# Performance work log

Hardware: AMD Instinct MI355X
Metric: run time of the kernel (lower is better)

## Reference

```python
import jax, jax.numpy as jnp
import numpy as np

IGNORE_THRESH = 0.75
COORD_SCALE = 1.0
NOOBJ_SCALE = 1.0
OBJ_SCALE = 5.0
CLASS_SCALE = 1.0


def setup_inputs() -> dict:
    key = jax.random.key(0)
    k1, k2, k3, k4, k5 = jax.random.split(key, 5)
    B, A, C, S, M = 32, 5, 20, 52, 50
    outputs = jax.random.normal(k1, (B, A * (5 + C), S, S), dtype=jnp.float32) * 0.5
    # targets: [x_c, y_c, w, h, conf, class] with normalized coords in (0,1)
    xy = jax.random.uniform(k2, (B, M, 2), minval=0.1, maxval=0.9)
    wh = jax.random.uniform(k3, (B, M, 2), minval=0.02, maxval=0.25)
    cls = jax.random.randint(k4, (B, M, 1), 0, C).astype(jnp.float32)
    conf = jnp.ones((B, M, 1), dtype=jnp.float32)
    targets = jnp.concatenate([xy, wh, conf, cls], axis=-1).astype(jnp.float32)
    anchors = jnp.array([[1.3221, 1.73145], [3.19275, 4.00944], [5.05587, 8.09892],
                         [9.47112, 4.84053], [11.2364, 10.0071]], dtype=jnp.float32)
    return {"outputs": outputs, "targets": targets, "anchors": anchors}


def _iou_xywh(a, b):
    # a: [B, N, 4], b: [B, M, 4] (cx, cy, w, h) -> [B, N, M]
    tl = jnp.maximum(a[:, :, None, :2] - a[:, :, None, 2:] * 0.5,
                     b[:, None, :, :2] - b[:, None, :, 2:] * 0.5)
    br = jnp.minimum(a[:, :, None, :2] + a[:, :, None, 2:] * 0.5,
                     b[:, None, :, :2] + b[:, None, :, 2:] * 0.5)
    en = jnp.all(tl < br, axis=-1).astype(a.dtype)
    area_i = jnp.prod(br - tl, axis=-1) * en
    area_a = a[:, :, 2] * a[:, :, 3]
    area_b = b[:, :, 2] * b[:, :, 3]
    return area_i / (area_a[:, :, None] + area_b[:, None, :] - area_i)


def _yolo_loss(outputs, targets, anchors):
    B, Ct, S, _ = outputs.shape
    A = anchors.shape[0]
    nc = Ct // A - 5
    dt = outputs.dtype
    out = outputs.reshape(B, A, 5 + nc, S, S).transpose(0, 1, 3, 4, 2)  # B,A,S,S,D

    # ---- decode predicted boxes (grid units) ----
    xs = jnp.arange(S, dtype=dt)
    px = jax.nn.sigmoid(out[..., 0]) + xs[None, None, None, :]
    py = jax.nn.sigmoid(out[..., 1]) + xs[None, None, :, None]
    pw = jnp.exp(out[..., 2]) * anchors[:, 0][None, :, None, None]
    ph = jnp.exp(out[..., 3]) * anchors[:, 1][None, :, None, None]
    # cell-major ordering: (S*S, A)
    pred_boxes = jnp.stack([px, py, pw, ph], -1).transpose(0, 2, 3, 1, 4).reshape(B, S * S * A, 4)

    valid = targets.sum(-1) > 0                      # [B,M]
    gt = targets[..., :4] * S                        # [B,M,4] grid units
    gcls = targets[..., 5].astype(jnp.int32)         # [B,M]

    # ---- pred-vs-gt IoU, ignore mask ----
    ious = _iou_xywh(pred_boxes, gt)                 # [B, S*S*A, M]
    ious = jnp.where(valid[:, None, :], ious, 0.0)
    max_iou = ious.max(-1).reshape(B, S * S, A)      # [B,S*S,A]
    iou_mask = jnp.where(max_iou >= IGNORE_THRESH, 0.0, NOOBJ_SCALE).astype(dt)

    # ---- per-gt responsible cell & anchor ----
    gx, gy, gw, gh = gt[..., 0], gt[..., 1], gt[..., 2], gt[..., 3]
    cx = jnp.clip(jnp.floor(gx - gw * 0.5), 0, S - 1).astype(jnp.int32)
    cy = jnp.clip(jnp.floor(gy - gh * 0.5), 0, S - 1).astype(jnp.int32)
    cell = cy * S + cx                               # [B,M]
    acx = cx.astype(dt) + 0.5
    acy = cy.astype(dt) + 0.5
    aw, ah = anchors[:, 0], anchors[:, 1]            # [A]
    # anchor-vs-gt IoU at the responsible cell: [B,M,A]
    tlx = jnp.maximum(acx[..., None] - aw * 0.5, (gx - gw * 0.5)[..., None])
    brx = jnp.minimum(acx[..., None] + aw * 0.5, (gx + gw * 0.5)[..., None])
    tly = jnp.maximum(acy[..., None] - ah * 0.5, (gy - gh * 0.5)[..., None])
    bry = jnp.minimum(acy[..., None] + ah * 0.5, (gy + gh * 0.5)[..., None])
    en = ((tlx < brx) & (tly < bry)).astype(dt)
    inter = (brx - tlx) * (bry - tly) * en
    aiou = inter / (aw * ah + (gw * gh)[..., None] - inter)
    best = jnp.argmax(aiou, -1)                      # [B,M]

    # deltas sigma(tx), sigma(ty), exp(tw), exp(th)
    deltas = jnp.stack([gx - acx, gy - acy, gw / aw[best], gh / ah[best]], -1)  # [B,M,4]

    b_idx = jnp.broadcast_to(jnp.arange(B)[:, None], cell.shape)
    cell_sc = jnp.where(valid, cell, S * S)          # OOB -> dropped on scatter
    miou = max_iou[b_idx, cell, best]                # [B,M]

    box_target = jnp.zeros((B, S * S, A, 4), dt).at[b_idx, cell_sc, best].set(deltas)
    box_mask = jnp.zeros((B, S * S, A), dt).at[b_idx, cell_sc, best].set(1.0)
    class_target = jnp.zeros((B, S * S, A), jnp.int32).at[b_idx, cell_sc, best].set(gcls)
    class_mask = jnp.zeros((B, S * S, A), dt).at[b_idx, cell_sc, best].set(1.0)
    iou_target = jnp.zeros((B, S * S, A), dt).at[b_idx, cell_sc, best].set(miou)
    iou_mask = iou_mask.at[b_idx, cell_sc, best].set(OBJ_SCALE)

    # ---- losses (cell-major predictions) ----
    pr = out.transpose(0, 2, 3, 1, 4).reshape(B, S * S, A, 5 + nc)
    pred_delta = jnp.concatenate([jax.nn.sigmoid(pr[..., :2]), jnp.exp(pr[..., 2:4])], -1)
    pconf = jax.nn.sigmoid(pr[..., 4])
    logp = jax.nn.log_softmax(pr[..., 5:], axis=-1)

    Bf = jnp.asarray(B, dt)
    box_loss = COORD_SCALE * jnp.sum(box_mask[..., None] * (pred_delta - box_target) ** 2) / (2.0 * Bf)
    iou_loss = jnp.sum((iou_mask * (pconf - iou_target)) ** 2) / (2.0 * Bf)
    nll = -jnp.take_along_axis(logp, class_target[..., None], axis=-1)[..., 0]
    class_loss = CLASS_SCALE * jnp.sum(class_mask * nll) / Bf
    return box_loss + iou_loss + class_loss


def reference(outputs, targets, anchors):
    return _yolo_loss(outputs, targets, anchors)
```

## Files before the change

### kernel.cpp

```cpp
#include <hip/hip_runtime.h>
#include <math.h>

namespace {
constexpr int S  = 52;
constexpr int SS = S * S;
constexpr int A  = 5;
constexpr int NC = 20;
constexpr int CH = 5 + NC;
constexpr int B  = 32;
constexpr int M  = 50;
constexpr int TSTRIDE = 6;
constexpr float IGNORE_T = 0.75f;
constexpr float C37 = 3.0f / 7.0f;

constexpr int POS_PER_T = 4;
constexpr int CHUNK = 256 * POS_PER_T;
constexpr int NBY = (SS + CHUNK - 1) / CHUNK;
constexpr int NBA = B * A;
constexpr int NBLK_NOOBJ = NBA * NBY;
constexpr int NBLK = NBLK_NOOBJ + B;
constexpr int Q4 = SS / 4;

__device__ __forceinline__ float sigm(float x) { return 1.0f / (1.0f + __expf(-x)); }

__device__ __forceinline__ float iou_one(float px, float py, float pw, float ph,
                                         float gx, float gy, float gw, float gh) {
  float tlx = fmaxf(px - pw * 0.5f, gx - gw * 0.5f);
  float brx = fminf(px + pw * 0.5f, gx + gw * 0.5f);
  float tly = fmaxf(py - ph * 0.5f, gy - gh * 0.5f);
  float bry = fminf(py + ph * 0.5f, gy + gh * 0.5f);
  if (tlx < brx && tly < bry) {
    float ai = (brx - tlx) * (bry - tly);
    return ai / (pw * ph + gw * gh - ai);
  }
  return 0.0f;
}

__global__ __launch_bounds__(256) void k_fused(const float* __restrict__ outp,
                                               const float* __restrict__ targ,
                                               const float* __restrict__ anch,
                                               float* __restrict__ out) {
  __shared__ float4 sgc[M];
  __shared__ float  sga[M];
  __shared__ float  sg[M][4];
  __shared__ int    sv[M];
  __shared__ int    skey[64];
  __shared__ float  wsum[4];

  const int bid = blockIdx.x;
  const int tid = threadIdx.x;

  if (bid < NBLK_NOOBJ) {
    const int ba = bid % NBA;
    const int by = bid / NBA;
    const int b  = ba / A, a = ba % A;
    if (tid < M) {
      const float* t = targ + (size_t)(b * M + tid) * TSTRIDE;
      float t0 = t[0], t1 = t[1], t2 = t[2], t3 = t[3], t4 = t[4], t5 = t[5];
      bool valid = (t0 + t1 + t2 + t3 + t4 + t5) > 0.0f;
      float gx = t0 * S, gy = t1 * S, gw = t2 * S, gh = t3 * S;
      if (valid) {
        sgc[tid] = make_float4(gx - gw * 0.5f, gy - gh * 0.5f,
                               gx + gw * 0.5f, gy + gh * 0.5f);
        sga[tid] = C37 * gw * gh;
      } else {
        sgc[tid] = make_float4(1e30f, 1e30f, -1e30f, -1e30f);
        sga[tid] = 0.0f;
      }
    }
    __syncthreads();

    const float aw = anch[2 * a], ah = anch[2 * a + 1];
    int q = by * (CHUNK / 4) + tid;
    const bool act = q < Q4;
    if (!act) q = Q4 - 1;
    const float4* p0 = (const float4*)(outp + (size_t)ba * CH * SS);
    float4 tx4 = p0[q];
    float4 ty4 = p0[q + Q4];
    float4 tw4 = p0[q + 2 * Q4];
    float4 th4 = p0[q + 3 * Q4];
    float4 tc4 = p0[q + 4 * Q4];

    const int pos0 = q * 4;
    const int y = pos0 / S, x0 = pos0 - y * S;
    const float fy = (float)y;

    float ptlx[POS_PER_T], ptly[POS_PER_T], pbrx[POS_PER_T], pbry[POS_PER_T];
    float rhsb[POS_PER_T], pcsq[POS_PER_T];
    const float txx[4] = {tx4.x, tx4.y, tx4.z, tx4.w};
    const float tyy[4] = {ty4.x, ty4.y, ty4.z, ty4.w};
    const float tww[4] = {tw4.x, tw4.y, tw4.z, tw4.w};
    const float thh[4] = {th4.x, th4.y, th4.z, th4.w};
    const float tcc[4] = {tc4.x, tc4.y, tc4.z, tc4.w};
#pragma unroll
    for (int k = 0; k < POS_PER_T; ++k) {
      float px = sigm(txx[k]) + (float)(x0 + k);
      float py = sigm(tyy[k]) + fy;
      float pw = __expf(tww[k]) * aw;
      float ph = __expf(thh[k]) * ah;
      float hw = pw * 0.5f, hh = ph * 0.5f;
      ptlx[k] = px - hw;
      ptly[k] = py - hh;
      pbrx[k] = px + hw;
      pbry[k] = py + hh;
      rhsb[k] = C37 * (pw * ph);
      float pc = sigm(tcc[k]);
      pcsq[k] = act ? pc * pc : 0.0f;
    }

    for (int m = 0; m < M; ++m) {
      float4 g = sgc[m];
      float ga = sga[m];
#pragma unroll
      for (int k = 0; k < POS_PER_T; ++k) {
        float dx = fminf(pbrx[k], g.z) - fmaxf(ptlx[k], g.x);
        float dy = fminf(pbry[k], g.w) - fmaxf(ptly[k], g.y);
        float ai = dx * dy;
        bool hit = (fminf(dx, dy) > 0.0f) & (ai >= rhsb[k] + ga);
        pcsq[k] = hit ? 0.0f : pcsq[k];
      }
    }

    float term = (pcsq[0] + pcsq[1]) + (pcsq[2] + pcsq[3]);
    for (int off = 32; off > 0; off >>= 1) term += __shfl_down(term, off);
    int lane = tid & 63, wid = tid >> 6;
    if (lane == 0) wsum[wid] = term;
    __syncthreads();
    if (tid == 0)
      atomicAdd(out, (wsum[0] + wsum[1] + wsum[2] + wsum[3]) * (1.0f / 64.0f));
  } else {
    const int b = bid - NBLK_NOOBJ;
    const int m = tid;
    int valid = 0;
    float gx = 0, gy = 0, gw = 0, gh = 0;
    int gcls = 0, cx = 0, cy = 0, best = 0;
    float dxv = 0, dyv = 0, dwv = 0, dhv = 0;
    if (m < M) {
      const float* t = targ + (size_t)(b * M + m) * TSTRIDE;
      float t0 = t[0], t1 = t[1], t2 = t[2], t3 = t[3], t4 = t[4], t5 = t[5];
      valid = (t0 + t1 + t2 + t3 + t4 + t5) > 0.0f ? 1 : 0;
      gx = t0 * S; gy = t1 * S; gw = t2 * S; gh = t3 * S;
      gcls = (int)t5;
      sg[m][0] = gx; sg[m][1] = gy; sg[m][2] = gw; sg[m][3] = gh;
      sv[m] = valid;
    }
    if (valid) {
      cx = (int)fminf(fmaxf(floorf(gx - gw * 0.5f), 0.0f), (float)(S - 1));
      cy = (int)fminf(fmaxf(floorf(gy - gh * 0.5f), 0.0f), (float)(S - 1));
      float acx = cx + 0.5f, acy = cy + 0.5f;
      float bestv = -1.0f;
      for (int k = 0; k < A; ++k) {
        float aw = anch[2 * k], ah = anch[2 * k + 1];
        float tlx = fmaxf(acx - aw * 0.5f, gx - gw * 0.5f);
        float brx = fminf(acx + aw * 0.5f, gx + gw * 0.5f);
        float tly = fmaxf(acy - ah * 0.5f, gy - gh * 0.5f);
        float bry = fminf(acy + ah * 0.5f, gy + gh * 0.5f);
        float v = 0.0f;
        if (tlx < brx && tly < bry) {
          float ai = (brx - tlx) * (bry - tly);
          v = ai / (aw * ah + gw * gh - ai);
        }
        if (v > bestv) { bestv = v; best = k; }
      }
      dxv = gx - acx; dyv = gy - acy;
      dwv = gw / anch[2 * best]; dhv = gh / anch[2 * best + 1];
    }
    if (m < 64) skey[m] = valid ? ((cy * S + cx) * A + best) : -1;
    __syncthreads();
    bool winner = (valid != 0);
    if (winner) {
      int key = skey[m];
      for (int mm = m + 1; mm < M; ++mm)
        if (skey[mm] == key) { winner = false; break; }
    }
    float ciou = 0.0f, cbox = 0.0f, ccls = 0.0f;
    if (winner) {
      int cell = cy * S + cx;
      const float* base = outp + (size_t)(b * A + best) * CH * SS + cell;
      float tx = base[0], ty = base[SS], tw = base[2 * SS], th = base[3 * SS], tc = base[4 * SS];
      float aw = anch[2 * best], ah = anch[2 * best + 1];
      float px = sigm(tx) + (float)cx;
      float py = sigm(ty) + (float)cy;
      float pw = __expf(tw) * aw;
      float ph = __expf(th) * ah;
      float miou = 0.0f;
      for (int mm = 0; mm < M; ++mm)
        if (sv[mm])
          miou = fmaxf(miou, iou_one(px, py, pw, ph,
                                     sg[mm][0], sg[mm][1], sg[mm][2], sg[mm][3]));
      float pc = sigm(tc);
      float defterm = (miou >= IGNORE_T) ? 0.0f : pc * pc;
      float d5 = 5.0f * (pc - miou);
      ciou = d5 * d5 - defterm;
      float e0 = sigm(tx) - dxv;
      float e1 = sigm(ty) - dyv;
      float e2 = __expf(tw) - dwv;
      float e3 = __expf(th) - dhv;
      cbox = e0 * e0 + e1 * e1 + e2 * e2 + e3 * e3;
      float l[NC];
      float lmax = -1e30f;
      for (int c = 0; c < NC; ++c) { l[c] = base[(5 + c) * SS]; lmax = fmaxf(lmax, l[c]); }
      float se = 0.0f;
      for (int c = 0; c < NC; ++c) se += __expf(l[c] - lmax);
      ccls = (lmax + __logf(se)) - l[gcls];
    }
    if (m < 64) {
      for (int off = 32; off > 0; off >>= 1) {
        ciou += __shfl_down(ciou, off);
        cbox += __shfl_down(cbox, off);
        ccls += __shfl_down(ccls, off);
      }
      if (m == 0)
        atomicAdd(out, (ciou + cbox) * (1.0f / 64.0f) + ccls * (1.0f / 32.0f));
    }
  }
}

}

extern "C" void kernel_launch(void* const* d_in, const int* in_sizes, int n_in,
                              void* d_out, int out_size, void* d_ws, size_t ws_size,
                              hipStream_t stream) {
  const float* outp = (const float*)d_in[0];
  const float* targ = (const float*)d_in[1];
  const float* anch = (const float*)d_in[2];

  hipMemsetAsync(d_out, 0, 4, stream);
  k_fused<<<NBLK, 256, 0, stream>>>(outp, targ, anch, (float*)d_out);
}
```

Before: 31.38 us.

## Replace memset and global atomics with flag-based last-block reduction in block zero

Removes the separate hipMemsetAsync on the output and the 512 atomicAdds that all hit one address. Each producer block now writes its partial sum to a workspace slot and publishes a release flag. Block 0 spin-waits on all 512 flags, reduces the partials, writes the result directly and resets the flags. This saves a launch and the atomic contention. In exchange it relies on every block being co-resident or making progress while block 0 spins, and on the workspace flags starting out not equal to the magic value.

```diff
diff --git a/kernel.cpp b/kernel.cpp
--- a/kernel.cpp
+++ b/kernel.cpp
@@ -18,8 +18,10 @@
 constexpr int NBY = (SS + CHUNK - 1) / CHUNK;
 constexpr int NBA = B * A;
 constexpr int NBLK_NOOBJ = NBA * NBY;
-constexpr int NBLK = NBLK_NOOBJ + B;
+constexpr int NPROD = NBLK_NOOBJ + B;
+constexpr int NBLK = NPROD + 1;
 constexpr int Q4 = SS / 4;
+constexpr unsigned MAGIC = 0x5F3759DFu;
 
 __device__ __forceinline__ float sigm(float x) { return 1.0f / (1.0f + __expf(-x)); }
 
@@ -36,9 +38,18 @@
   return 0.0f;
 }
 
+__device__ __forceinline__ void publish(float* partials, unsigned* flags, int p,
+                                        float v) {
+  partials[p] = v;
+  __threadfence();
+  __hip_atomic_store(&flags[p], MAGIC, __ATOMIC_RELEASE, __HIP_MEMORY_SCOPE_AGENT);
+}
+
 __global__ __launch_bounds__(256) void k_fused(const float* __restrict__ outp,
                                                const float* __restrict__ targ,
                                                const float* __restrict__ anch,
+                                               float* __restrict__ partials,
+                                               unsigned* __restrict__ flags,
                                                float* __restrict__ out) {
   __shared__ float4 sgc[M];
   __shared__ float  sga[M];
@@ -50,9 +61,34 @@
   const int bid = blockIdx.x;
   const int tid = threadIdx.x;
 
-  if (bid < NBLK_NOOBJ) {
-    const int ba = bid % NBA;
-    const int by = bid / NBA;
+  if (bid == 0) {
+    const int i0 = tid, i1 = tid + 256;
+    while (__hip_atomic_load(&flags[i0], __ATOMIC_ACQUIRE,
+                             __HIP_MEMORY_SCOPE_AGENT) != MAGIC)
+      __builtin_amdgcn_s_sleep(2);
+    while (__hip_atomic_load(&flags[i1], __ATOMIC_ACQUIRE,
+                             __HIP_MEMORY_SCOPE_AGENT) != MAGIC)
+      __builtin_amdgcn_s_sleep(2);
+    float s = __hip_atomic_load(&partials[i0], __ATOMIC_RELAXED,
+                                __HIP_MEMORY_SCOPE_AGENT) +
+              __hip_atomic_load(&partials[i1], __ATOMIC_RELAXED,
+                                __HIP_MEMORY_SCOPE_AGENT);
+    for (int off = 32; off > 0; off >>= 1) s += __shfl_down(s, off);
+    int lane = tid & 63, wid = tid >> 6;
+    if (lane == 0) wsum[wid] = s;
+    __syncthreads();
+    if (tid == 0)
+      out[0] = wsum[0] + wsum[1] + wsum[2] + wsum[3];
+    __hip_atomic_store(&flags[i0], 0u, __ATOMIC_RELAXED, __HIP_MEMORY_SCOPE_AGENT);
+    __hip_atomic_store(&flags[i1], 0u, __ATOMIC_RELAXED, __HIP_MEMORY_SCOPE_AGENT);
+    return;
+  }
+
+  const int p = bid - 1;
+
+  if (p < NBLK_NOOBJ) {
+    const int ba = p % NBA;
+    const int by = p / NBA;
     const int b  = ba / A, a = ba % A;
     if (tid < M) {
       const float* t = targ + (size_t)(b * M + tid) * TSTRIDE;
@@ -127,9 +163,10 @@
     if (lane == 0) wsum[wid] = term;
     __syncthreads();
     if (tid == 0)
-      atomicAdd(out, (wsum[0] + wsum[1] + wsum[2] + wsum[3]) * (1.0f / 64.0f));
+      publish(partials, flags, p,
+              (wsum[0] + wsum[1] + wsum[2] + wsum[3]) * (1.0f / 64.0f));
   } else {
-    const int b = bid - NBLK_NOOBJ;
+    const int b = p - NBLK_NOOBJ;
     const int m = tid;
     int valid = 0;
     float gx = 0, gy = 0, gw = 0, gh = 0;
@@ -211,7 +248,8 @@
         ccls += __shfl_down(ccls, off);
       }
       if (m == 0)
-        atomicAdd(out, (ciou + cbox) * (1.0f / 64.0f) + ccls * (1.0f / 32.0f));
+        publish(partials, flags, p,
+                (ciou + cbox) * (1.0f / 64.0f) + ccls * (1.0f / 32.0f));
     }
   }
 }
@@ -224,7 +262,9 @@
   const float* outp = (const float*)d_in[0];
   const float* targ = (const float*)d_in[1];
   const float* anch = (const float*)d_in[2];
-
-  hipMemsetAsync(d_out, 0, 4, stream);
-  k_fused<<<NBLK, 256, 0, stream>>>(outp, targ, anch, (float*)d_out);
-}
+  float*    partials = (float*)d_ws;
+  unsigned* flags    = (unsigned*)((float*)d_ws + NPROD);
+
+  k_fused<<<NBLK, 256, 0, stream>>>(outp, targ, anch, partials, flags,
+                                    (float*)d_out);
+}
```

After: 29.26 us. 1.07x faster.
